# Kernel tuning notes

Measured on AMD Instinct MI355X. Metric: run time of the kernel, lower is better.

Reference implementation:

```python
import jax, jax.numpy as jnp
import numpy as np

# S6Layer dims: d_model=256; internal d_state=max(8,16//2)=8; expand=max(1.5,2*0.75)=1.5 -> d_inner=384
B, L, DM = 8, 4096, 256
DI, DS = 384, 8
CHUNK = 32  # seq_len > 64 path: chunked scan, state resets to 0 at every chunk (faithful to source)
EPS = 1e-5


def setup_inputs() -> dict:
    key = jax.random.key(0)
    ks = jax.random.split(key, 8)
    def w(k, shape, s=0.02):
        return jax.random.normal(k, shape, jnp.float32) * s
    return {
        "x": jax.random.normal(ks[0], (B, L, DM), jnp.float32),
        "gamma": jnp.ones((DM,), jnp.float32),
        "beta": jnp.zeros((DM,), jnp.float32),
        "W_in": w(ks[1], (3 * DI, DM)),
        "b_in": jnp.zeros((3 * DI,), jnp.float32),
        "W_dt": w(ks[2], (DI, DI)),
        "b_dt": jnp.zeros((DI,), jnp.float32),
        "A_log": jax.random.normal(ks[3], (DI, DS), jnp.float32),
        "D_vec": jax.random.normal(ks[4], (DI,), jnp.float32),
        "W_out": w(ks[5], (DM, DI)),
        "b_out": jnp.zeros((DM,), jnp.float32),
    }


def _layernorm(x, g, b):
    mu = jnp.mean(x, axis=-1, keepdims=True)
    var = jnp.mean(jnp.square(x - mu), axis=-1, keepdims=True)
    return (x - mu) * jax.lax.rsqrt(var + EPS) * g + b


def _chunked_scan(xp, dt, A):
    # xp, dt: [B, L, DI]; A: [DI, DS]. Each CHUNK-length block scans from h=0
    # (the torch code never propagates h across chunks for seq_len > 64).
    C = L // CHUNK
    xr = xp.reshape(B, C, CHUNK, DI)
    dtr = dt.reshape(B, C, CHUNK, DI)
    dA = jnp.exp(dtr[..., None] * A)              # [B, C, T, DI, DS]
    dA_t = jnp.moveaxis(dA, 2, 0)                 # [T, B, C, DI, DS]
    x_t = jnp.moveaxis(xr, 2, 0)                  # [T, B, C, DI]

    def step(h, inp):
        dA_i, x_i = inp
        h = h * dA_i + x_i[..., None]             # broadcast x over DS
        return h, jnp.sum(h, axis=-1)             # y_i: [B, C, DI]

    h0 = jnp.zeros((B, C, DI, DS), xp.dtype)
    _, ys = jax.lax.scan(step, h0, (dA_t, x_t))   # ys: [T, B, C, DI]
    return jnp.moveaxis(ys, 0, 2).reshape(B, L, DI)


def reference(x, gamma, beta, W_in, b_in, W_dt, b_dt, A_log, D_vec, W_out, b_out):
    residual = x
    xn = _layernorm(x, gamma, beta)
    xz = xn @ W_in.T + b_in                       # [B, L, 3*DI]
    x_proj, z, dt_in = jnp.split(xz, 3, axis=-1)
    x_proj = jax.nn.silu(x_proj)
    z = jax.nn.silu(z)
    dt = jax.nn.softplus(dt_in @ W_dt.T + b_dt)   # [B, L, DI]
    A = -jnp.exp(A_log)                           # [DI, DS]
    y = _chunked_scan(x_proj, dt, A)
    y = y * z + x_proj * D_vec
    return y @ W_out.T + b_out + residual
```

## Files before the change

### kernel.cpp

```cpp
#include <hip/hip_runtime.h>
#include <stdint.h>

#define B_  8
#define L_  4096
#define DM  256
#define DI  384
#define DS  8
#define M_  (B_*L_)

typedef float f32x4 __attribute__((ext_vector_type(4)));
typedef short s16x8 __attribute__((ext_vector_type(8)));

#define AS1(p) ((__attribute__((address_space(1))) void*)(p))
#define AS3(p) ((__attribute__((address_space(3))) void*)(p))

__device__ __forceinline__ unsigned short f2bf(float f) {
  union { float f; uint32_t u; } v; v.f = f;
  uint32_t r = v.u + 0x7FFFu + ((v.u >> 16) & 1u);
  return (unsigned short)(r >> 16);
}
__device__ __forceinline__ float bf2f(unsigned short h) {
  union { uint32_t u; float f; } v; v.u = ((uint32_t)h) << 16;
  return v.f;
}
__device__ __forceinline__ float silu_f(float x) { return x / (1.f + __expf(-x)); }

__global__ __launch_bounds__(256) void cvt_kernel(
    const float* __restrict__ w0, const float* __restrict__ w1, const float* __restrict__ w2,
    unsigned short* __restrict__ o0, unsigned short* __restrict__ o1, unsigned short* __restrict__ o2) {
  int i = blockIdx.x * 256 + threadIdx.x;
  if (i < 3*DI*DM) o0[i] = f2bf(w0[i]);
  if (i < DI*DI)   o1[i] = f2bf(w1[i]);
  if (i < DM*DI)   o2[i] = f2bf(w2[i]);
}

__global__ __launch_bounds__(256) void ln_kernel(
    const float* __restrict__ x, const float* __restrict__ gamma, const float* __restrict__ beta,
    unsigned short* __restrict__ xn) {
  int token = blockIdx.x * 4 + (threadIdx.x >> 6);
  int lane  = threadIdx.x & 63;
  const float4 v = *(const float4*)(x + (size_t)token*DM + lane*4);
  float s  = v.x + v.y + v.z + v.w;
  float ss = v.x*v.x + v.y*v.y + v.z*v.z + v.w*v.w;
  #pragma unroll
  for (int off = 32; off > 0; off >>= 1) {
    s  += __shfl_xor(s,  off, 64);
    ss += __shfl_xor(ss, off, 64);
  }
  float mean = s * (1.f/DM);
  float var  = ss * (1.f/DM) - mean*mean;
  float rstd = rsqrtf(var + 1e-5f);
  const float4 g = *(const float4*)(gamma + lane*4);
  const float4 b = *(const float4*)(beta  + lane*4);
  ushort4 o;
  o.x = f2bf((v.x - mean)*rstd*g.x + b.x);
  o.y = f2bf((v.y - mean)*rstd*g.y + b.y);
  o.z = f2bf((v.z - mean)*rstd*g.z + b.z);
  o.w = f2bf((v.w - mean)*rstd*g.w + b.w);
  *(ushort4*)(xn + (size_t)token*DM + lane*4) = o;
}

template<int EPI, int KSTEPS>
__global__ __launch_bounds__(256, 2) void gemm_ws(
    const unsigned short* __restrict__ A,
    const unsigned short* __restrict__ Bw,
    const float* __restrict__ bias,
    unsigned short* __restrict__ o_xp, unsigned short* __restrict__ o_z,
    unsigned short* __restrict__ o_dtin,
    unsigned short* __restrict__ o_bf,
    const float* __restrict__ resid, float* __restrict__ o_f)
{
  constexpr int K    = KSTEPS * 32;
  constexpr int CPR  = K / 8;
  constexpr int SM_E = 64*K + 8192;
  __shared__ unsigned short smem[SM_E];
  unsigned short* sB = smem;

  const int t    = threadIdx.x;
  const int lane = t & 63;
  const int w    = t >> 6;
  const int fr   = lane & 15;
  const int fq   = lane >> 4;
  const int mbase = blockIdx.x * 128;
  const int nbase = blockIdx.y * 64;
  const int wm   = w * 32;
  unsigned short* sAw = smem + 64*K + w*2048;

  #pragma unroll
  for (int i = 0; i < (64*CPR)/256; ++i) {
    int c   = i*256 + t;
    int row = c / CPR;
    int j   = c - row*CPR;
    int jp  = (j & ~7) | ((j & 7) ^ (row & 7));
    __builtin_amdgcn_global_load_lds(AS1(Bw + (size_t)(nbase + row)*K + jp*8),
                                     AS3(sB + c*8), 16, 0, 0);
  }

  const unsigned short* gA[2];
  #pragma unroll
  for (int i = 0; i < 2; ++i)
    gA[i] = A + (size_t)(mbase + wm + i*16 + (lane >> 2)) * K + (lane & 3)*8;

  #pragma unroll
  for (int i = 0; i < 2; ++i)
    __builtin_amdgcn_global_load_lds(AS1(gA[i]), AS3(sAw + i*512), 16, 0, 0);

  f32x4 acc[2][4];
  #pragma unroll
  for (int mi = 0; mi < 2; ++mi)
    #pragma unroll
    for (int ni = 0; ni < 4; ++ni) acc[mi][ni] = (f32x4){0.f, 0.f, 0.f, 0.f};

  __syncthreads();

  #pragma unroll
  for (int kt = 0; kt < KSTEPS; ++kt) {
    __builtin_amdgcn_sched_barrier(0);
    if (kt + 1 < KSTEPS) {
      unsigned short* dstb = sAw + ((kt+1) & 1)*1024;
      #pragma unroll
      for (int i = 0; i < 2; ++i)
        __builtin_amdgcn_global_load_lds(AS1(gA[i] + (kt+1)*32), AS3(dstb + i*512), 16, 0, 0);
      asm volatile("s_waitcnt vmcnt(2)" ::: "memory");
    } else {
      asm volatile("s_waitcnt vmcnt(0)" ::: "memory");
    }
    __builtin_amdgcn_sched_barrier(0);
    const unsigned short* rbuf = sAw + (kt & 1)*1024;
    s16x8 af[2], bfr[4];
    #pragma unroll
    for (int mi = 0; mi < 2; ++mi)
      af[mi] = *(const s16x8*)(rbuf + mi*512 + fr*32 + fq*8);
    #pragma unroll
    for (int ni = 0; ni < 4; ++ni) {
      int r    = ni*16 + fr;
      int j    = kt*4 + fq;
      int slot = (j & ~7) | ((j & 7) ^ (r & 7));
      bfr[ni]  = *(const s16x8*)(sB + r*K + slot*8);
    }
    #pragma unroll
    for (int mi = 0; mi < 2; ++mi)
      #pragma unroll
      for (int ni = 0; ni < 4; ++ni)
        acc[mi][ni] = __builtin_amdgcn_mfma_f32_16x16x32_bf16(af[mi], bfr[ni], acc[mi][ni], 0, 0, 0);
  }

  if constexpr (EPI == 3) {
    #pragma unroll
    for (int ni = 0; ni < 4; ++ni) {
      int gn = nbase + ni*16 + fr;
      float bv = bias[gn];
      #pragma unroll
      for (int mi = 0; mi < 2; ++mi) {
        int gm0 = mbase + wm + mi*16 + fq*4;
        #pragma unroll
        for (int r = 0; r < 4; ++r) {
          size_t gm = (size_t)(gm0 + r);
          o_f[gm*DM + gn] = acc[mi][ni][r] + bv + resid[gm*DM + gn];
        }
      }
    }
  } else {
    __syncthreads();
    const bool do_silu = (EPI == 1) && (blockIdx.y < 12);
    #pragma unroll
    for (int ni = 0; ni < 4; ++ni) {
      int cn = ni*16 + fr;
      float bv = bias[nbase + cn];
      #pragma unroll
      for (int mi = 0; mi < 2; ++mi) {
        int rm0 = wm + mi*16 + fq*4;
        #pragma unroll
        for (int r = 0; r < 4; ++r) {
          float c = acc[mi][ni][r] + bv;
          if constexpr (EPI == 1) { if (do_silu) c = silu_f(c); }
          else                    { c = (c > 20.f) ? c : log1pf(__expf(c)); }
          smem[(rm0 + r)*72 + cn] = f2bf(c);
        }
      }
    }
    __syncthreads();
    unsigned short* dst;
    int colbase;
    if constexpr (EPI == 1) {
      int p = blockIdx.y;
      dst = (p < 6) ? o_xp : (p < 12) ? o_z : o_dtin;
      colbase = (p % 6) * 64;
    } else {
      dst = o_bf; colbase = nbase;
    }
    const int rr = t >> 3, cc = (t & 7) * 8;
    #pragma unroll
    for (int it = 0; it < 4; ++it) {
      int row = rr + it*32;
      s16x8 v = *(const s16x8*)(smem + row*72 + cc);
      *(s16x8*)(dst + (size_t)(mbase + row)*DI + colbase + cc) = v;
    }
  }
}

__global__ __launch_bounds__(384) void scan_kernel(
    const unsigned short* __restrict__ xp, const unsigned short* __restrict__ dt,
    const unsigned short* __restrict__ zb, const float* __restrict__ A_log,
    const float* __restrict__ D_vec, unsigned short* __restrict__ yz) {
  int g  = blockIdx.x;
  int di = threadIdx.x;
  size_t base = (size_t)g * 32 * DI + di;
  float a[DS];
  #pragma unroll
  for (int s = 0; s < DS; ++s) a[s] = -__expf(A_log[di*DS + s]);
  float Dv = D_vec[di];
  float h[DS] = {0.f,0.f,0.f,0.f,0.f,0.f,0.f,0.f};
  for (int tt = 0; tt < 32; ++tt) {
    size_t idx = base + (size_t)tt * DI;
    float xv  = bf2f(xp[idx]);
    float dtv = bf2f(dt[idx]);
    float y = 0.f;
    #pragma unroll
    for (int s = 0; s < DS; ++s) {
      h[s] = h[s] * __expf(dtv * a[s]) + xv;
      y += h[s];
    }
    float zv = bf2f(zb[idx]);
    yz[idx] = f2bf(y * zv + xv * Dv);
  }
}

extern "C" void kernel_launch(void* const* d_in, const int* in_sizes, int n_in,
                              void* d_out, int out_size, void* d_ws, size_t ws_size,
                              hipStream_t stream) {
  const float* x     = (const float*)d_in[0];
  const float* gamma = (const float*)d_in[1];
  const float* beta  = (const float*)d_in[2];
  const float* W_in  = (const float*)d_in[3];
  const float* b_in  = (const float*)d_in[4];
  const float* W_dt  = (const float*)d_in[5];
  const float* b_dt  = (const float*)d_in[6];
  const float* A_log = (const float*)d_in[7];
  const float* D_vec = (const float*)d_in[8];
  const float* W_out = (const float*)d_in[9];
  const float* b_out = (const float*)d_in[10];
  float* out = (float*)d_out;

  char* ws = (char*)d_ws;
  size_t off = 0;
  auto alloc = [&](size_t bytes) -> char* {
    char* p = ws + off; off += (bytes + 255) & ~(size_t)255; return p;
  };
  unsigned short* xn    = (unsigned short*)alloc((size_t)M_*DM*2);
  unsigned short* xpb   = (unsigned short*)alloc((size_t)M_*DI*2);
  unsigned short* zb    = (unsigned short*)alloc((size_t)M_*DI*2);
  unsigned short* dtin  = (unsigned short*)alloc((size_t)M_*DI*2);
  unsigned short* dtb   = (unsigned short*)alloc((size_t)M_*DI*2);
  unsigned short* yzb   = dtin;
  unsigned short* winb  = (unsigned short*)alloc((size_t)3*DI*DM*2);
  unsigned short* wdtb  = (unsigned short*)alloc((size_t)DI*DI*2);
  unsigned short* woutb = (unsigned short*)alloc((size_t)DM*DI*2);

  cvt_kernel<<<dim3((3*DI*DM + 255)/256), 256, 0, stream>>>(W_in, W_dt, W_out, winb, wdtb, woutb);
  ln_kernel<<<dim3(M_/4), 256, 0, stream>>>(x, gamma, beta, xn);
  gemm_ws<1, 8><<<dim3(M_/128, (3*DI)/64), 256, 0, stream>>>(
      xn, winb, b_in, xpb, zb, dtin, nullptr, nullptr, nullptr);
  gemm_ws<2, 12><<<dim3(M_/128, DI/64), 256, 0, stream>>>(
      dtin, wdtb, b_dt, nullptr, nullptr, nullptr, dtb, nullptr, nullptr);
  scan_kernel<<<dim3(M_/32), DI, 0, stream>>>(xpb, dtb, zb, A_log, D_vec, yzb);
  gemm_ws<3, 12><<<dim3(M_/128, DM/64), 256, 0, stream>>>(
      yzb, woutb, b_out, nullptr, nullptr, nullptr, nullptr, x, out);
}
```

Before: 242.8 us.

## Load GEMM A fragments directly from global and raise occupancy

The GEMM kernel no longer stages A tiles through double-buffered LDS with async global-to-LDS copies and manual waitcnt. Each lane now loads its MFMA A fragment straight from global memory into registers. This shrinks the shared-memory footprint, which allows the launch bound to go from 2 to 3 blocks per CU. The swizzled B fragment addresses are precomputed as even/odd base pointers, and softplus uses the fast `__logf` instead of `log1pf`. The trade-off is that explicit prefetch overlap is lost, global loads become less coalesced, and register pressure rises under the tighter launch bound.

```diff
diff --git a/kernel.cpp b/kernel.cpp
--- a/kernel.cpp
+++ b/kernel.cpp
@@ -61,7 +61,7 @@
 }
 
 template<int EPI, int KSTEPS>
-__global__ __launch_bounds__(256, 2) void gemm_ws(
+__global__ __launch_bounds__(256, 3) void gemm_ws(
     const unsigned short* __restrict__ A,
     const unsigned short* __restrict__ Bw,
     const float* __restrict__ bias,
@@ -72,8 +72,7 @@
 {
   constexpr int K    = KSTEPS * 32;
   constexpr int CPR  = K / 8;
-  constexpr int SM_E = 64*K + 8192;
-  __shared__ unsigned short smem[SM_E];
+  __shared__ unsigned short smem[64*K];
   unsigned short* sB = smem;
 
   const int t    = threadIdx.x;
@@ -84,7 +83,6 @@
   const int mbase = blockIdx.x * 128;
   const int nbase = blockIdx.y * 64;
   const int wm   = w * 32;
-  unsigned short* sAw = smem + 64*K + w*2048;
 
   #pragma unroll
   for (int i = 0; i < (64*CPR)/256; ++i) {
@@ -96,14 +94,11 @@
                                      AS3(sB + c*8), 16, 0, 0);
   }
 
-  const unsigned short* gA[2];
-  #pragma unroll
-  for (int i = 0; i < 2; ++i)
-    gA[i] = A + (size_t)(mbase + wm + i*16 + (lane >> 2)) * K + (lane & 3)*8;
-
-  #pragma unroll
-  for (int i = 0; i < 2; ++i)
-    __builtin_amdgcn_global_load_lds(AS1(gA[i]), AS3(sAw + i*512), 16, 0, 0);
+  const unsigned short* gA0 = A + (size_t)(mbase + wm + fr)*K + fq*8;
+  const unsigned short* gA1 = gA0 + (size_t)16*K;
+
+  const unsigned short* sBrE = sB + (size_t)fr*K + ( fq      ^ (fr & 7))*8;
+  const unsigned short* sBrO = sB + (size_t)fr*K + ((fq | 4) ^ (fr & 7))*8;
 
   f32x4 acc[2][4];
   #pragma unroll
@@ -115,34 +110,18 @@
 
   #pragma unroll
   for (int kt = 0; kt < KSTEPS; ++kt) {
-    __builtin_amdgcn_sched_barrier(0);
-    if (kt + 1 < KSTEPS) {
-      unsigned short* dstb = sAw + ((kt+1) & 1)*1024;
-      #pragma unroll
-      for (int i = 0; i < 2; ++i)
-        __builtin_amdgcn_global_load_lds(AS1(gA[i] + (kt+1)*32), AS3(dstb + i*512), 16, 0, 0);
-      asm volatile("s_waitcnt vmcnt(2)" ::: "memory");
-    } else {
-      asm volatile("s_waitcnt vmcnt(0)" ::: "memory");
-    }
-    __builtin_amdgcn_sched_barrier(0);
-    const unsigned short* rbuf = sAw + (kt & 1)*1024;
-    s16x8 af[2], bfr[4];
-    #pragma unroll
-    for (int mi = 0; mi < 2; ++mi)
-      af[mi] = *(const s16x8*)(rbuf + mi*512 + fr*32 + fq*8);
+    s16x8 af0 = *(const s16x8*)(gA0 + kt*32);
+    s16x8 af1 = *(const s16x8*)(gA1 + kt*32);
+    const unsigned short* bb = (kt & 1) ? sBrO : sBrE;
+    s16x8 bfr[4];
+    #pragma unroll
+    for (int ni = 0; ni < 4; ++ni)
+      bfr[ni] = *(const s16x8*)(bb + ni*16*K + (kt >> 1)*64);
     #pragma unroll
     for (int ni = 0; ni < 4; ++ni) {
-      int r    = ni*16 + fr;
-      int j    = kt*4 + fq;
-      int slot = (j & ~7) | ((j & 7) ^ (r & 7));
-      bfr[ni]  = *(const s16x8*)(sB + r*K + slot*8);
-    }
-    #pragma unroll
-    for (int mi = 0; mi < 2; ++mi)
-      #pragma unroll
-      for (int ni = 0; ni < 4; ++ni)
-        acc[mi][ni] = __builtin_amdgcn_mfma_f32_16x16x32_bf16(af[mi], bfr[ni], acc[mi][ni], 0, 0, 0);
+      acc[0][ni] = __builtin_amdgcn_mfma_f32_16x16x32_bf16(af0, bfr[ni], acc[0][ni], 0, 0, 0);
+      acc[1][ni] = __builtin_amdgcn_mfma_f32_16x16x32_bf16(af1, bfr[ni], acc[1][ni], 0, 0, 0);
+    }
   }
 
   if constexpr (EPI == 3) {
@@ -174,7 +153,7 @@
         for (int r = 0; r < 4; ++r) {
           float c = acc[mi][ni][r] + bv;
           if constexpr (EPI == 1) { if (do_silu) c = silu_f(c); }
-          else                    { c = (c > 20.f) ? c : log1pf(__expf(c)); }
+          else                    { c = (c > 20.f) ? c : __logf(1.f + __expf(c)); }
           smem[(rm0 + r)*72 + cn] = f2bf(c);
         }
       }
```

After: 226.6 us. -6.7%, faster.
